# Performance work log

Hardware: AMD Instinct MI355X
Metric: run time of the kernel (lower is better)

## Reference

```python
import jax, jax.numpy as jnp
import numpy as np

N = 100000   # nodes
E = 1600000  # edges
D = 128      # emb_dim == in_dim
L = 5        # num_layer
G = 128      # graphs in batch
T = 10       # num_tasks
NB = 4       # edge (bond) types
BN_EPS = 1e-5


def setup_inputs() -> dict:
    key = jax.random.key(0)
    ks = jax.random.split(key, 10)
    x = jax.random.normal(ks[0], (N, D), jnp.float32)
    edge_index = jax.random.randint(ks[1], (2, E), 0, N, dtype=jnp.int32)
    edge_attr = jax.random.randint(ks[2], (E,), 0, NB, dtype=jnp.int32)
    batch = jnp.sort(jax.random.randint(ks[3], (N,), 0, G, dtype=jnp.int32))
    # stacked per-layer params (layer 0 has in_dim == emb_dim == D)
    W = jax.random.normal(ks[4], (L, D, D), jnp.float32) * 0.05
    b = jnp.zeros((L, D), jnp.float32)
    root = jax.random.normal(ks[5], (L, D), jnp.float32) * 0.05   # root_emb.weight per layer
    bond = jax.random.normal(ks[6], (L, NB, D), jnp.float32) * 0.05  # bond encoder tables
    gamma = jnp.ones((L, D), jnp.float32)
    beta = jnp.zeros((L, D), jnp.float32)
    W_out = jax.random.normal(ks[7], (D, T), jnp.float32) * 0.05
    b_out = jnp.zeros((T,), jnp.float32)
    return {"x": x, "edge_index": edge_index, "edge_attr": edge_attr, "batch": batch,
            "W": W, "b": b, "root": root, "bond": bond, "gamma": gamma, "beta": beta,
            "W_out": W_out, "b_out": b_out}


def reference(x, edge_index, edge_attr, batch, W, b, root, bond, gamma, beta, W_out, b_out):
    row, col = edge_index[0], edge_index[1]
    # degree of source nodes (+1 self), symmetric-ish norm as in GCNConv.forward
    deg = jax.ops.segment_sum(jnp.ones((E,), x.dtype), row, num_segments=N) + 1.0  # [N]
    dinv = deg ** -0.5  # never inf since deg >= 1
    norm = dinv[row] * dinv[col]  # [E]
    h = x
    for l in range(L):
        hx = h @ W[l] + b[l]                                   # [N, D] linear
        ee = bond[l][edge_attr]                                # [E, D] edge embedding gather
        msg = norm[:, None] * jax.nn.relu(hx[row] + ee)        # [E, D] message
        agg = jax.ops.segment_sum(msg, col, num_segments=N)    # [N, D] scatter-add to targets
        h2 = agg + jax.nn.relu(hx + root[l]) / deg[:, None]    # self/root term
        # BatchNorm1d (training-mode batch stats, biased variance)
        mu = h2.mean(axis=0)
        var = h2.var(axis=0)
        h2 = (h2 - mu) * jax.lax.rsqrt(var + BN_EPS) * gamma[l] + beta[l]
        h = jax.nn.relu(h2)
    # global mean pool over graphs
    cnt = jnp.maximum(jax.ops.segment_sum(jnp.ones((N,), h.dtype), batch, num_segments=G), 1.0)
    hg = jax.ops.segment_sum(h, batch, num_segments=G) / cnt[:, None]  # [G, D]
    return hg @ W_out + b_out  # [G, T]
```

## Files before the change

### kernel.cpp

```cpp
#include <hip/hip_runtime.h>
#include <hip/hip_fp16.h>
#include <math.h>

#define N_NODES 100000
#define N_EDGES 1600000
#define DIM     128
#define NLAYER  5
#define NGRAPH  128
#define NTASK   10
#define NBOND   4
#define BN_EPS  1e-5f

__global__ __launch_bounds__(256) void hist_kernel(
    const int* __restrict__ row, const int* __restrict__ col,
    int* __restrict__ cnt_row, int* __restrict__ cnt_col) {
  int i = blockIdx.x * blockDim.x + threadIdx.x;
  int stride = gridDim.x * blockDim.x;
  for (; i < N_EDGES; i += stride) {
    atomicAdd(&cnt_row[row[i]], 1);
    atomicAdd(&cnt_col[col[i]], 1);
  }
}

__global__ __launch_bounds__(256) void deg_kernel(
    const int* __restrict__ cnt_row, float* __restrict__ deg, float* __restrict__ dinv) {
  int i = blockIdx.x * blockDim.x + threadIdx.x;
  if (i < N_NODES) {
    float d = (float)cnt_row[i] + 1.0f;
    deg[i] = d;
    dinv[i] = rsqrtf(d);
  }
}

__global__ __launch_bounds__(256) void scan1_kernel(
    const int* __restrict__ cnt, int* __restrict__ excl, int* __restrict__ bsum) {
  __shared__ int s[256];
  int t = threadIdx.x;
  int i = blockIdx.x * 256 + t;
  int v = (i < N_NODES) ? cnt[i] : 0;
  s[t] = v;
  __syncthreads();
  for (int off = 1; off < 256; off <<= 1) {
    int add = (t >= off) ? s[t - off] : 0;
    __syncthreads();
    s[t] += add;
    __syncthreads();
  }
  if (i < N_NODES) excl[i] = s[t] - v;
  if (t == 255) bsum[blockIdx.x] = s[255];
}

__global__ __launch_bounds__(512) void scan2_kernel(
    const int* __restrict__ bsum, int* __restrict__ bexcl, int nb) {
  __shared__ int s[512];
  int t = threadIdx.x;
  int v = (t < nb) ? bsum[t] : 0;
  s[t] = v;
  __syncthreads();
  for (int off = 1; off < 512; off <<= 1) {
    int add = (t >= off) ? s[t - off] : 0;
    __syncthreads();
    s[t] += add;
    __syncthreads();
  }
  if (t < nb) bexcl[t] = s[t] - v;
}

__global__ __launch_bounds__(256) void scan3_kernel(
    int* __restrict__ excl, const int* __restrict__ bexcl) {
  int i = blockIdx.x * 256 + threadIdx.x;
  if (i < N_NODES) excl[i] += bexcl[blockIdx.x];
  if (i == 0) excl[N_NODES] = N_EDGES;
}

__global__ __launch_bounds__(256) void scatter_kernel(
    const int* __restrict__ row, const int* __restrict__ col,
    const int* __restrict__ attr, const int* __restrict__ csr_off,
    int* __restrict__ pos, const float* __restrict__ dinv,
    int* __restrict__ src_pack, float* __restrict__ enorm) {
  int e = blockIdx.x * blockDim.x + threadIdx.x;
  int stride = gridDim.x * blockDim.x;
  for (; e < N_EDGES; e += stride) {
    int d = col[e];
    int s = row[e];
    int p = csr_off[d] + atomicAdd(&pos[d], 1);
    src_pack[p] = s | (attr[e] << 20);
    enorm[p] = dinv[s] * dinv[d];
  }
}

__device__ __forceinline__ void bn_coeff(float s, float q, float g, float b,
                                         float& sc, float& sh) {
  const float invN = 1.0f / (float)N_NODES;
  float mu = s * invN;
  float ex2 = q * invN;
  float var = ex2 - mu * mu;
  float inv = rsqrtf(var + BN_EPS);
  sc = g * inv;
  sh = fmaf(-mu, sc, b);
}

__device__ __forceinline__ void bn_coeff4(float4 s, float4 q, float4 g, float4 b,
                                          float4& sc, float4& sh) {
  bn_coeff(s.x, q.x, g.x, b.x, sc.x, sh.x);
  bn_coeff(s.y, q.y, g.y, b.y, sc.y, sh.y);
  bn_coeff(s.z, q.z, g.z, b.z, sc.z, sh.z);
  bn_coeff(s.w, q.w, g.w, b.w, sc.w, sh.w);
}

#define GBM 128
__global__ __launch_bounds__(512, 4) void gemm_kernel(
    const float* __restrict__ hin, const float* __restrict__ W,
    const float* __restrict__ bias, const float* __restrict__ bnprev,
    const float* __restrict__ gammaL, const float* __restrict__ betaL,
    int useact, uint2* __restrict__ hxh, float* __restrict__ bnzero) {
  __shared__ float4 hs[128 * 8];
  __shared__ float4 Ws[32 * 32];
  int t = threadIdx.x;
  if (blockIdx.x == 0 && t < 256) bnzero[t] = 0.0f;
  int cg = t & 15;
  int rg = t >> 4;
  int cr = rg & 3;
  int slot = t & 7;
  int srow = t >> 3;
  int sswz = slot ^ (srow & 3);
  int r0 = blockIdx.x * GBM;
  if (r0 > N_NODES - GBM) r0 = N_NODES - GBM;

  const float4* hg = (const float4*)hin;
  const float4* wg = (const float4*)W;
  const float4* bs4 = (const float4*)bnprev;
  const float4* g4 = (const float4*)gammaL;
  const float4* b4 = (const float4*)betaL;

  float acc0[4][4], acc1[4][4];
  {
    float b0[4], b1[4];
#pragma unroll
    for (int j = 0; j < 4; j++) {
      b0[j] = bias[4 * cg + j];
      b1[j] = bias[64 + 4 * cg + j];
    }
#pragma unroll
    for (int i = 0; i < 4; i++)
#pragma unroll
      for (int j = 0; j < 4; j++) { acc0[i][j] = b0[j]; acc1[i][j] = b1[j]; }
  }

  float4 psc, psh;
  if (useact) {
    float4 s4 = bs4[slot], q4 = bs4[32 + slot];
    bn_coeff4(s4, q4, g4[slot], b4[slot], psc, psh);
  }
  float4 ph0 = hg[(size_t)(r0 + srow) * 32 + slot];
  float4 ph1 = hg[(size_t)(r0 + srow + 64) * 32 + slot];
  float4 pw0 = wg[t];
  float4 pw1 = wg[512 + t];

#pragma unroll 1
  for (int p = 0; p < 4; ++p) {
    float4 v0 = ph0, v1 = ph1;
    if (useact) {
      v0.x = fmaxf(fmaf(v0.x, psc.x, psh.x), 0.f);
      v0.y = fmaxf(fmaf(v0.y, psc.y, psh.y), 0.f);
      v0.z = fmaxf(fmaf(v0.z, psc.z, psh.z), 0.f);
      v0.w = fmaxf(fmaf(v0.w, psc.w, psh.w), 0.f);
      v1.x = fmaxf(fmaf(v1.x, psc.x, psh.x), 0.f);
      v1.y = fmaxf(fmaf(v1.y, psc.y, psh.y), 0.f);
      v1.z = fmaxf(fmaf(v1.z, psc.z, psh.z), 0.f);
      v1.w = fmaxf(fmaf(v1.w, psc.w, psh.w), 0.f);
    }
    hs[srow * 8 + sswz] = v0;
    hs[(srow + 64) * 8 + sswz] = v1;
    Ws[t] = pw0;
    Ws[512 + t] = pw1;
    __syncthreads();
    if (p < 3) {
      if (useact) {
        float4 s4 = bs4[(p + 1) * 8 + slot], q4 = bs4[32 + (p + 1) * 8 + slot];
        bn_coeff4(s4, q4, g4[(p + 1) * 8 + slot], b4[(p + 1) * 8 + slot], psc, psh);
      }
      ph0 = hg[(size_t)(r0 + srow) * 32 + (p + 1) * 8 + slot];
      ph1 = hg[(size_t)(r0 + srow + 64) * 32 + (p + 1) * 8 + slot];
      pw0 = wg[(p + 1) * 1024 + t];
      pw1 = wg[(p + 1) * 1024 + 512 + t];
    }
#pragma unroll 1
    for (int k4 = 0; k4 < 8; k4++) {
      float4 w0[4], w1[4];
#pragma unroll
      for (int kk = 0; kk < 4; kk++) {
        w0[kk] = Ws[(k4 * 4 + kk) * 32 + cg];
        w1[kk] = Ws[(k4 * 4 + kk) * 32 + 16 + cg];
      }
      int soff = k4 ^ cr;
#pragma unroll
      for (int i = 0; i < 4; i++) {
        float4 hf = hs[(rg + 32 * i) * 8 + soff];
#pragma unroll
        for (int kk = 0; kk < 4; kk++) {
          float hv = ((const float*)&hf)[kk];
          acc0[i][0] = fmaf(hv, w0[kk].x, acc0[i][0]);
          acc0[i][1] = fmaf(hv, w0[kk].y, acc0[i][1]);
          acc0[i][2] = fmaf(hv, w0[kk].z, acc0[i][2]);
          acc0[i][3] = fmaf(hv, w0[kk].w, acc0[i][3]);
          acc1[i][0] = fmaf(hv, w1[kk].x, acc1[i][0]);
          acc1[i][1] = fmaf(hv, w1[kk].y, acc1[i][1]);
          acc1[i][2] = fmaf(hv, w1[kk].z, acc1[i][2]);
          acc1[i][3] = fmaf(hv, w1[kk].w, acc1[i][3]);
        }
      }
    }
    __syncthreads();
  }
#pragma unroll
  for (int i = 0; i < 4; i++) {
    int grow = r0 + rg + 32 * i;
    __half2 a01 = __floats2half2_rn(acc0[i][0], acc0[i][1]);
    __half2 a23 = __floats2half2_rn(acc0[i][2], acc0[i][3]);
    __half2 c01 = __floats2half2_rn(acc1[i][0], acc1[i][1]);
    __half2 c23 = __floats2half2_rn(acc1[i][2], acc1[i][3]);
    uint2 u0, u1;
    u0.x = __builtin_bit_cast(unsigned int, a01);
    u0.y = __builtin_bit_cast(unsigned int, a23);
    u1.x = __builtin_bit_cast(unsigned int, c01);
    u1.y = __builtin_bit_cast(unsigned int, c23);
    hxh[(size_t)grow * 32 + cg] = u0;
    hxh[(size_t)grow * 32 + 16 + cg] = u1;
  }
}

__global__ __launch_bounds__(256) void agg_kernel(
    const uint2* __restrict__ hxh, const int* __restrict__ csr_off,
    const int* __restrict__ src_pack, const float* __restrict__ enorm,
    const float* __restrict__ bond, const float* __restrict__ root,
    const float* __restrict__ deg, float* __restrict__ h2,
    float* __restrict__ bnbuf) {
  __shared__ float4 bondS[NBOND * 32];
  __shared__ float4 rootS[32];
  __shared__ float sbn[256];
  int t = threadIdx.x;
  if (t < NBOND * 32) bondS[t] = ((const float4*)bond)[t];
  if (t < 32) rootS[t] = ((const float4*)root)[t];
  sbn[t] = 0.0f;
  __syncthreads();

  int lane = t & 63;
  int laneq = lane & 31;
  int half = lane >> 5;
  int wid = t >> 6;
  int gw = blockIdx.x * 4 + wid;
  int nw = gridDim.x * 4;
  float4* h24 = (float4*)h2;

  float s0 = 0.f, s1 = 0.f, s2 = 0.f, s3 = 0.f;
  float q0 = 0.f, q1 = 0.f, q2 = 0.f, q3 = 0.f;
  for (int n = gw; n < N_NODES; n += nw) {
    int e0 = csr_off[n], e1 = csr_off[n + 1];
    float a0 = 0.f, a1 = 0.f, a2 = 0.f, a3 = 0.f;
    int e = e0 + half;
    for (; e + 6 < e1; e += 8) {
      int sp0 = src_pack[e];
      int sp1 = src_pack[e + 2];
      int sp2 = src_pack[e + 4];
      int sp3 = src_pack[e + 6];
      float nr0 = enorm[e];
      float nr1 = enorm[e + 2];
      float nr2 = enorm[e + 4];
      float nr3 = enorm[e + 6];
      uint2 u0 = hxh[(size_t)(sp0 & 0xFFFFF) * 32 + laneq];
      uint2 u1 = hxh[(size_t)(sp1 & 0xFFFFF) * 32 + laneq];
      uint2 u2 = hxh[(size_t)(sp2 & 0xFFFFF) * 32 + laneq];
      uint2 u3 = hxh[(size_t)(sp3 & 0xFFFFF) * 32 + laneq];
      float4 b0 = bondS[(sp0 >> 20) * 32 + laneq];
      float4 b1 = bondS[(sp1 >> 20) * 32 + laneq];
      float4 b2 = bondS[(sp2 >> 20) * 32 + laneq];
      float4 b3 = bondS[(sp3 >> 20) * 32 + laneq];
      float2 v0a = __half22float2(__builtin_bit_cast(__half2, u0.x));
      float2 v0b = __half22float2(__builtin_bit_cast(__half2, u0.y));
      float2 v1a = __half22float2(__builtin_bit_cast(__half2, u1.x));
      float2 v1b = __half22float2(__builtin_bit_cast(__half2, u1.y));
      float2 v2a = __half22float2(__builtin_bit_cast(__half2, u2.x));
      float2 v2b = __half22float2(__builtin_bit_cast(__half2, u2.y));
      float2 v3a = __half22float2(__builtin_bit_cast(__half2, u3.x));
      float2 v3b = __half22float2(__builtin_bit_cast(__half2, u3.y));
      a0 = fmaf(nr0, fmaxf(v0a.x + b0.x, 0.f), a0);
      a1 = fmaf(nr0, fmaxf(v0a.y + b0.y, 0.f), a1);
      a2 = fmaf(nr0, fmaxf(v0b.x + b0.z, 0.f), a2);
      a3 = fmaf(nr0, fmaxf(v0b.y + b0.w, 0.f), a3);
      a0 = fmaf(nr1, fmaxf(v1a.x + b1.x, 0.f), a0);
      a1 = fmaf(nr1, fmaxf(v1a.y + b1.y, 0.f), a1);
      a2 = fmaf(nr1, fmaxf(v1b.x + b1.z, 0.f), a2);
      a3 = fmaf(nr1, fmaxf(v1b.y + b1.w, 0.f), a3);
      a0 = fmaf(nr2, fmaxf(v2a.x + b2.x, 0.f), a0);
      a1 = fmaf(nr2, fmaxf(v2a.y + b2.y, 0.f), a1);
      a2 = fmaf(nr2, fmaxf(v2b.x + b2.z, 0.f), a2);
      a3 = fmaf(nr2, fmaxf(v2b.y + b2.w, 0.f), a3);
      a0 = fmaf(nr3, fmaxf(v3a.x + b3.x, 0.f), a0);
      a1 = fmaf(nr3, fmaxf(v3a.y + b3.y, 0.f), a1);
      a2 = fmaf(nr3, fmaxf(v3b.x + b3.z, 0.f), a2);
      a3 = fmaf(nr3, fmaxf(v3b.y + b3.w, 0.f), a3);
    }
    for (; e < e1; e += 2) {
      int sp = src_pack[e];
      float nrm = enorm[e];
      uint2 u = hxh[(size_t)(sp & 0xFFFFF) * 32 + laneq];
      float4 eb = bondS[(sp >> 20) * 32 + laneq];
      float2 va = __half22float2(__builtin_bit_cast(__half2, u.x));
      float2 vb = __half22float2(__builtin_bit_cast(__half2, u.y));
      a0 = fmaf(nrm, fmaxf(va.x + eb.x, 0.f), a0);
      a1 = fmaf(nrm, fmaxf(va.y + eb.y, 0.f), a1);
      a2 = fmaf(nrm, fmaxf(vb.x + eb.z, 0.f), a2);
      a3 = fmaf(nrm, fmaxf(vb.y + eb.w, 0.f), a3);
    }
    a0 += __shfl_xor(a0, 32, 64);
    a1 += __shfl_xor(a1, 32, 64);
    a2 += __shfl_xor(a2, 32, 64);
    a3 += __shfl_xor(a3, 32, 64);
    if (half == 0) {
      float inv = 1.0f / deg[n];
      uint2 u = hxh[(size_t)n * 32 + laneq];
      float2 va = __half22float2(__builtin_bit_cast(__half2, u.x));
      float2 vb = __half22float2(__builtin_bit_cast(__half2, u.y));
      float4 r = rootS[laneq];
      a0 += fmaxf(va.x + r.x, 0.f) * inv;
      a1 += fmaxf(va.y + r.y, 0.f) * inv;
      a2 += fmaxf(vb.x + r.z, 0.f) * inv;
      a3 += fmaxf(vb.y + r.w, 0.f) * inv;
      float4 o;
      o.x = a0; o.y = a1; o.z = a2; o.w = a3;
      h24[(size_t)n * 32 + laneq] = o;
      s0 += a0; s1 += a1; s2 += a2; s3 += a3;
      q0 += a0 * a0; q1 += a1 * a1; q2 += a2 * a2; q3 += a3 * a3;
    }
  }
  if (half == 0) {
    int f = 4 * laneq;
    atomicAdd(&sbn[f + 0], s0);
    atomicAdd(&sbn[f + 1], s1);
    atomicAdd(&sbn[f + 2], s2);
    atomicAdd(&sbn[f + 3], s3);
    atomicAdd(&sbn[128 + f + 0], q0);
    atomicAdd(&sbn[128 + f + 1], q1);
    atomicAdd(&sbn[128 + f + 2], q2);
    atomicAdd(&sbn[128 + f + 3], q3);
  }
  __syncthreads();
  atomicAdd(&bnbuf[t], sbn[t]);
}

__global__ __launch_bounds__(256) void pool_kernel(
    const float* __restrict__ h2, const int* __restrict__ batch,
    const float* __restrict__ bnlast, const float* __restrict__ gammaL,
    const float* __restrict__ betaL,
    float* __restrict__ pool, float* __restrict__ pcnt) {
  int t = threadIdx.x;
  int lane = t & 63;
  int wid = t >> 6;
  int gw = blockIdx.x * 4 + wid;
  int nw = gridDim.x * 4;
  int chunk = (N_NODES + nw - 1) / nw;
  int n0 = gw * chunk;
  int n1 = min(n0 + chunk, N_NODES);
  if (n0 >= N_NODES) return;
  const float2* h22 = (const float2*)h2;
  int f0 = 2 * lane, f1 = f0 + 1;
  float sc0, sh0, sc1, sh1;
  bn_coeff(bnlast[f0], bnlast[128 + f0], gammaL[f0], betaL[f0], sc0, sh0);
  bn_coeff(bnlast[f1], bnlast[128 + f1], gammaL[f1], betaL[f1], sc1, sh1);
  int curg = batch[n0];
  float a0 = 0.f, a1 = 0.f, c = 0.f;
  for (int n = n0; n < n1; n++) {
    int g = batch[n];
    if (g != curg) {
      atomicAdd(&pool[curg * DIM + f0], a0);
      atomicAdd(&pool[curg * DIM + f1], a1);
      if (lane == 0) atomicAdd(&pcnt[curg], c);
      a0 = a1 = c = 0.f;
      curg = g;
    }
    float2 v = h22[(size_t)n * 64 + lane];
    a0 += fmaxf(fmaf(v.x, sc0, sh0), 0.f);
    a1 += fmaxf(fmaf(v.y, sc1, sh1), 0.f);
    c += 1.0f;
  }
  atomicAdd(&pool[curg * DIM + f0], a0);
  atomicAdd(&pool[curg * DIM + f1], a1);
  if (lane == 0) atomicAdd(&pcnt[curg], c);
}

__global__ __launch_bounds__(256) void out_kernel(
    const float* __restrict__ pool, const float* __restrict__ pcnt,
    const float* __restrict__ Wout, const float* __restrict__ bout,
    float* __restrict__ out) {
  int idx = blockIdx.x * blockDim.x + threadIdx.x;
  if (idx >= NGRAPH * NTASK) return;
  int g = idx / NTASK, tt = idx % NTASK;
  float inv = 1.0f / fmaxf(pcnt[g], 1.0f);
  float acc = bout[tt];
  for (int d = 0; d < DIM; d++)
    acc = fmaf(pool[g * DIM + d] * inv, Wout[d * NTASK + tt], acc);
  out[idx] = acc;
}

extern "C" void kernel_launch(void* const* d_in, const int* in_sizes, int n_in,
                              void* d_out, int out_size, void* d_ws, size_t ws_size,
                              hipStream_t stream) {
  const float* x     = (const float*)d_in[0];
  const int*   eidx  = (const int*)d_in[1];
  const int*   row   = eidx;
  const int*   col   = eidx + N_EDGES;
  const int*   eattr = (const int*)d_in[2];
  const int*   batch = (const int*)d_in[3];
  const float* W     = (const float*)d_in[4];
  const float* b     = (const float*)d_in[5];
  const float* root  = (const float*)d_in[6];
  const float* bond  = (const float*)d_in[7];
  const float* gamma = (const float*)d_in[8];
  const float* beta  = (const float*)d_in[9];
  const float* Wout  = (const float*)d_in[10];
  const float* bout  = (const float*)d_in[11];
  float* out = (float*)d_out;

  char* w = (char*)d_ws;
  size_t off = 0;
  auto alloc = [&](size_t bytes) -> void* {
    void* p = w + off;
    off = (off + bytes + 511) & ~(size_t)511;
    return p;
  };
  int*   cnt_row = (int*)alloc(N_NODES * 4);
  int*   cnt_col = (int*)alloc(N_NODES * 4);
  int*   pos     = (int*)alloc(N_NODES * 4);
  float* pool    = (float*)alloc(NGRAPH * DIM * 4);
  float* pcnt    = (float*)alloc(NGRAPH * 4);
  size_t zbytes  = off;
  int*   csr     = (int*)alloc((N_NODES + 1) * 4);
  int*   bsum    = (int*)alloc(512 * 4);
  int*   bexcl   = (int*)alloc(512 * 4);
  float* deg     = (float*)alloc(N_NODES * 4);
  float* dinv    = (float*)alloc(N_NODES * 4);
  int*   spck    = (int*)alloc((size_t)N_EDGES * 4);
  float* enorm   = (float*)alloc((size_t)N_EDGES * 4);
  uint2* hxh     = (uint2*)alloc((size_t)N_NODES * DIM * 2);
  float* hA      = (float*)alloc((size_t)N_NODES * DIM * 4);
  float* hB      = (float*)alloc((size_t)N_NODES * DIM * 4);
  float* bnbufA  = (float*)alloc(256 * 4);
  float* bnbufB  = (float*)alloc(256 * 4);

  hipMemsetAsync(d_ws, 0, zbytes, stream);

  hist_kernel<<<2048, 256, 0, stream>>>(row, col, cnt_row, cnt_col);
  deg_kernel<<<(N_NODES + 255) / 256, 256, 0, stream>>>(cnt_row, deg, dinv);
  const int nb = (N_NODES + 255) / 256;
  scan1_kernel<<<nb, 256, 0, stream>>>(cnt_col, csr, bsum);
  scan2_kernel<<<1, 512, 0, stream>>>(bsum, bexcl, nb);
  scan3_kernel<<<nb, 256, 0, stream>>>(csr, bexcl);
  scatter_kernel<<<2048, 256, 0, stream>>>(row, col, eattr, csr, pos, dinv, spck, enorm);

  const int gblocks = (N_NODES + GBM - 1) / GBM;
  const float* hin = x;
  for (int l = 0; l < NLAYER; l++) {
    float* h2      = (l % 2 == 0) ? hA : hB;
    float* bufcur  = (l % 2 == 0) ? bnbufA : bnbufB;
    float* bufprev = (l % 2 == 0) ? bnbufB : bnbufA;
    gemm_kernel<<<gblocks, 512, 0, stream>>>(
        hin, W + (size_t)l * DIM * DIM, b + l * DIM,
        bufprev, gamma + (size_t)(l > 0 ? l - 1 : 0) * DIM,
        beta + (size_t)(l > 0 ? l - 1 : 0) * DIM,
        (l > 0) ? 1 : 0, hxh, bufcur);
    agg_kernel<<<2048, 256, 0, stream>>>(
        hxh, csr, spck, enorm, bond + (size_t)l * NBOND * DIM, root + l * DIM,
        deg, h2, bufcur);
    hin = h2;
  }
  pool_kernel<<<256, 256, 0, stream>>>(hin, batch, bnbufA,
                                       gamma + 4 * DIM, beta + 4 * DIM, pool, pcnt);
  out_kernel<<<5, 256, 0, stream>>>(pool, pcnt, Wout, bout, out);
}
```

Measured before the change: 1.224 ms.

## Fuse layer-0 GEMM with edge histogram, merge deg into scan, pack edge metadata

```diff
diff --git a/kernel.cpp b/kernel.cpp
--- a/kernel.cpp
+++ b/kernel.cpp
@@ -11,32 +11,17 @@
 #define NBOND   4
 #define BN_EPS  1e-5f
 
-__global__ __launch_bounds__(256) void hist_kernel(
-    const int* __restrict__ row, const int* __restrict__ col,
-    int* __restrict__ cnt_row, int* __restrict__ cnt_col) {
-  int i = blockIdx.x * blockDim.x + threadIdx.x;
-  int stride = gridDim.x * blockDim.x;
-  for (; i < N_EDGES; i += stride) {
-    atomicAdd(&cnt_row[row[i]], 1);
-    atomicAdd(&cnt_col[col[i]], 1);
-  }
-}
-
-__global__ __launch_bounds__(256) void deg_kernel(
+__global__ __launch_bounds__(256) void scan1_kernel(
+    const int* __restrict__ cnt, int* __restrict__ excl, int* __restrict__ bsum,
     const int* __restrict__ cnt_row, float* __restrict__ deg, float* __restrict__ dinv) {
-  int i = blockIdx.x * blockDim.x + threadIdx.x;
+  __shared__ int s[256];
+  int t = threadIdx.x;
+  int i = blockIdx.x * 256 + t;
   if (i < N_NODES) {
     float d = (float)cnt_row[i] + 1.0f;
     deg[i] = d;
     dinv[i] = rsqrtf(d);
   }
-}
-
-__global__ __launch_bounds__(256) void scan1_kernel(
-    const int* __restrict__ cnt, int* __restrict__ excl, int* __restrict__ bsum) {
-  __shared__ int s[256];
-  int t = threadIdx.x;
-  int i = blockIdx.x * 256 + t;
   int v = (i < N_NODES) ? cnt[i] : 0;
   s[t] = v;
   __syncthreads();
@@ -77,15 +62,17 @@
     const int* __restrict__ row, const int* __restrict__ col,
     const int* __restrict__ attr, const int* __restrict__ csr_off,
     int* __restrict__ pos, const float* __restrict__ dinv,
-    int* __restrict__ src_pack, float* __restrict__ enorm) {
+    int2* __restrict__ emeta) {
   int e = blockIdx.x * blockDim.x + threadIdx.x;
   int stride = gridDim.x * blockDim.x;
   for (; e < N_EDGES; e += stride) {
     int d = col[e];
     int s = row[e];
     int p = csr_off[d] + atomicAdd(&pos[d], 1);
-    src_pack[p] = s | (attr[e] << 20);
-    enorm[p] = dinv[s] * dinv[d];
+    int2 m;
+    m.x = s | (attr[e] << 20);
+    m.y = __float_as_int(dinv[s] * dinv[d]);
+    emeta[p] = m;
   }
 }
 
@@ -109,22 +96,20 @@
 }
 
 #define GBM 128
-__global__ __launch_bounds__(512, 4) void gemm_kernel(
+template<int USEACT>
+__device__ __forceinline__ void gemm_body(
     const float* __restrict__ hin, const float* __restrict__ W,
     const float* __restrict__ bias, const float* __restrict__ bnprev,
     const float* __restrict__ gammaL, const float* __restrict__ betaL,
-    int useact, uint2* __restrict__ hxh, float* __restrict__ bnzero) {
-  __shared__ float4 hs[128 * 8];
-  __shared__ float4 Ws[32 * 32];
-  int t = threadIdx.x;
-  if (blockIdx.x == 0 && t < 256) bnzero[t] = 0.0f;
+    uint2* __restrict__ hxh, float4* hs, float4* Ws, int bid) {
+  int t = threadIdx.x;
   int cg = t & 15;
   int rg = t >> 4;
   int cr = rg & 3;
   int slot = t & 7;
   int srow = t >> 3;
   int sswz = slot ^ (srow & 3);
-  int r0 = blockIdx.x * GBM;
+  int r0 = bid * GBM;
   if (r0 > N_NODES - GBM) r0 = N_NODES - GBM;
 
   const float4* hg = (const float4*)hin;
@@ -148,9 +133,8 @@
   }
 
   float4 psc, psh;
-  if (useact) {
-    float4 s4 = bs4[slot], q4 = bs4[32 + slot];
-    bn_coeff4(s4, q4, g4[slot], b4[slot], psc, psh);
+  if (USEACT) {
+    bn_coeff4(bs4[slot], bs4[32 + slot], g4[slot], b4[slot], psc, psh);
   }
   float4 ph0 = hg[(size_t)(r0 + srow) * 32 + slot];
   float4 ph1 = hg[(size_t)(r0 + srow + 64) * 32 + slot];
@@ -160,7 +144,7 @@
 #pragma unroll 1
   for (int p = 0; p < 4; ++p) {
     float4 v0 = ph0, v1 = ph1;
-    if (useact) {
+    if (USEACT) {
       v0.x = fmaxf(fmaf(v0.x, psc.x, psh.x), 0.f);
       v0.y = fmaxf(fmaf(v0.y, psc.y, psh.y), 0.f);
       v0.z = fmaxf(fmaf(v0.z, psc.z, psh.z), 0.f);
@@ -176,9 +160,9 @@
     Ws[512 + t] = pw1;
     __syncthreads();
     if (p < 3) {
-      if (useact) {
-        float4 s4 = bs4[(p + 1) * 8 + slot], q4 = bs4[32 + (p + 1) * 8 + slot];
-        bn_coeff4(s4, q4, g4[(p + 1) * 8 + slot], b4[(p + 1) * 8 + slot], psc, psh);
+      if (USEACT) {
+        bn_coeff4(bs4[(p + 1) * 8 + slot], bs4[32 + (p + 1) * 8 + slot],
+                  g4[(p + 1) * 8 + slot], b4[(p + 1) * 8 + slot], psc, psh);
       }
       ph0 = hg[(size_t)(r0 + srow) * 32 + (p + 1) * 8 + slot];
       ph1 = hg[(size_t)(r0 + srow + 64) * 32 + (p + 1) * 8 + slot];
@@ -230,9 +214,42 @@
   }
 }
 
+__global__ __launch_bounds__(512, 4) void gemm_kernel(
+    const float* __restrict__ hin, const float* __restrict__ W,
+    const float* __restrict__ bias, const float* __restrict__ bnprev,
+    const float* __restrict__ gammaL, const float* __restrict__ betaL,
+    uint2* __restrict__ hxh, float* __restrict__ bnzero) {
+  __shared__ float4 hs[128 * 8];
+  __shared__ float4 Ws[32 * 32];
+  if (blockIdx.x == 0 && threadIdx.x < 256) bnzero[threadIdx.x] = 0.0f;
+  gemm_body<1>(hin, W, bias, bnprev, gammaL, betaL, hxh, hs, Ws, blockIdx.x);
+}
+
+__global__ __launch_bounds__(512, 4) void gemm0_hist_kernel(
+    const float* __restrict__ x, const float* __restrict__ W,
+    const float* __restrict__ bias, uint2* __restrict__ hxh,
+    float* __restrict__ bnzero,
+    const int* __restrict__ row, const int* __restrict__ col,
+    int* __restrict__ cnt_row, int* __restrict__ cnt_col, int gblocks) {
+  __shared__ float4 hs[128 * 8];
+  __shared__ float4 Ws[32 * 32];
+  int t = threadIdx.x;
+  if ((int)blockIdx.x >= gblocks) {
+    int i = ((int)blockIdx.x - gblocks) * 512 + t;
+    int stride = ((int)gridDim.x - gblocks) * 512;
+    for (; i < N_EDGES; i += stride) {
+      atomicAdd(&cnt_row[row[i]], 1);
+      atomicAdd(&cnt_col[col[i]], 1);
+    }
+    return;
+  }
+  if (blockIdx.x == 0 && t < 256) bnzero[t] = 0.0f;
+  gemm_body<0>(x, W, bias, nullptr, nullptr, nullptr, hxh, hs, Ws, blockIdx.x);
+}
+
 __global__ __launch_bounds__(256) void agg_kernel(
     const uint2* __restrict__ hxh, const int* __restrict__ csr_off,
-    const int* __restrict__ src_pack, const float* __restrict__ enorm,
+    const int2* __restrict__ emeta,
     const float* __restrict__ bond, const float* __restrict__ root,
     const float* __restrict__ deg, float* __restrict__ h2,
     float* __restrict__ bnbuf) {
@@ -260,22 +277,22 @@
     float a0 = 0.f, a1 = 0.f, a2 = 0.f, a3 = 0.f;
     int e = e0 + half;
     for (; e + 6 < e1; e += 8) {
-      int sp0 = src_pack[e];
-      int sp1 = src_pack[e + 2];
-      int sp2 = src_pack[e + 4];
-      int sp3 = src_pack[e + 6];
-      float nr0 = enorm[e];
-      float nr1 = enorm[e + 2];
-      float nr2 = enorm[e + 4];
-      float nr3 = enorm[e + 6];
-      uint2 u0 = hxh[(size_t)(sp0 & 0xFFFFF) * 32 + laneq];
-      uint2 u1 = hxh[(size_t)(sp1 & 0xFFFFF) * 32 + laneq];
-      uint2 u2 = hxh[(size_t)(sp2 & 0xFFFFF) * 32 + laneq];
-      uint2 u3 = hxh[(size_t)(sp3 & 0xFFFFF) * 32 + laneq];
-      float4 b0 = bondS[(sp0 >> 20) * 32 + laneq];
-      float4 b1 = bondS[(sp1 >> 20) * 32 + laneq];
-      float4 b2 = bondS[(sp2 >> 20) * 32 + laneq];
-      float4 b3 = bondS[(sp3 >> 20) * 32 + laneq];
+      int2 m0 = emeta[e];
+      int2 m1 = emeta[e + 2];
+      int2 m2 = emeta[e + 4];
+      int2 m3 = emeta[e + 6];
+      float nr0 = __int_as_float(m0.y);
+      float nr1 = __int_as_float(m1.y);
+      float nr2 = __int_as_float(m2.y);
+      float nr3 = __int_as_float(m3.y);
+      uint2 u0 = hxh[(size_t)(m0.x & 0xFFFFF) * 32 + laneq];
+      uint2 u1 = hxh[(size_t)(m1.x & 0xFFFFF) * 32 + laneq];
+      uint2 u2 = hxh[(size_t)(m2.x & 0xFFFFF) * 32 + laneq];
+      uint2 u3 = hxh[(size_t)(m3.x & 0xFFFFF) * 32 + laneq];
+      float4 b0 = bondS[(m0.x >> 20) * 32 + laneq];
+      float4 b1 = bondS[(m1.x >> 20) * 32 + laneq];
+      float4 b2 = bondS[(m2.x >> 20) * 32 + laneq];
+      float4 b3 = bondS[(m3.x >> 20) * 32 + laneq];
       float2 v0a = __half22float2(__builtin_bit_cast(__half2, u0.x));
       float2 v0b = __half22float2(__builtin_bit_cast(__half2, u0.y));
       float2 v1a = __half22float2(__builtin_bit_cast(__half2, u1.x));
@@ -302,10 +319,10 @@
       a3 = fmaf(nr3, fmaxf(v3b.y + b3.w, 0.f), a3);
     }
     for (; e < e1; e += 2) {
-      int sp = src_pack[e];
-      float nrm = enorm[e];
-      uint2 u = hxh[(size_t)(sp & 0xFFFFF) * 32 + laneq];
-      float4 eb = bondS[(sp >> 20) * 32 + laneq];
+      int2 m = emeta[e];
+      float nrm = __int_as_float(m.y);
+      uint2 u = hxh[(size_t)(m.x & 0xFFFFF) * 32 + laneq];
+      float4 eb = bondS[(m.x >> 20) * 32 + laneq];
       float2 va = __half22float2(__builtin_bit_cast(__half2, u.x));
       float2 vb = __half22float2(__builtin_bit_cast(__half2, u.y));
       a0 = fmaf(nrm, fmaxf(va.x + eb.x, 0.f), a0);
@@ -440,8 +457,7 @@
   int*   bexcl   = (int*)alloc(512 * 4);
   float* deg     = (float*)alloc(N_NODES * 4);
   float* dinv    = (float*)alloc(N_NODES * 4);
-  int*   spck    = (int*)alloc((size_t)N_EDGES * 4);
-  float* enorm   = (float*)alloc((size_t)N_EDGES * 4);
+  int2*  emeta   = (int2*)alloc((size_t)N_EDGES * 8);
   uint2* hxh     = (uint2*)alloc((size_t)N_NODES * DIM * 2);
   float* hA      = (float*)alloc((size_t)N_NODES * DIM * 4);
   float* hB      = (float*)alloc((size_t)N_NODES * DIM * 4);
@@ -450,27 +466,30 @@
 
   hipMemsetAsync(d_ws, 0, zbytes, stream);
 
-  hist_kernel<<<2048, 256, 0, stream>>>(row, col, cnt_row, cnt_col);
-  deg_kernel<<<(N_NODES + 255) / 256, 256, 0, stream>>>(cnt_row, deg, dinv);
+  const int gblocks = (N_NODES + GBM - 1) / GBM;
+  gemm0_hist_kernel<<<gblocks + 512, 512, 0, stream>>>(
+      x, W, b, hxh, bnbufA, row, col, cnt_row, cnt_col, gblocks);
+
   const int nb = (N_NODES + 255) / 256;
-  scan1_kernel<<<nb, 256, 0, stream>>>(cnt_col, csr, bsum);
+  scan1_kernel<<<nb, 256, 0, stream>>>(cnt_col, csr, bsum, cnt_row, deg, dinv);
   scan2_kernel<<<1, 512, 0, stream>>>(bsum, bexcl, nb);
   scan3_kernel<<<nb, 256, 0, stream>>>(csr, bexcl);
-  scatter_kernel<<<2048, 256, 0, stream>>>(row, col, eattr, csr, pos, dinv, spck, enorm);
-
-  const int gblocks = (N_NODES + GBM - 1) / GBM;
-  const float* hin = x;
-  for (int l = 0; l < NLAYER; l++) {
+  scatter_kernel<<<2048, 256, 0, stream>>>(row, col, eattr, csr, pos, dinv, emeta);
+
+  agg_kernel<<<2048, 256, 0, stream>>>(
+      hxh, csr, emeta, bond, root, deg, hA, bnbufA);
+
+  const float* hin = hA;
+  for (int l = 1; l < NLAYER; l++) {
     float* h2      = (l % 2 == 0) ? hA : hB;
     float* bufcur  = (l % 2 == 0) ? bnbufA : bnbufB;
     float* bufprev = (l % 2 == 0) ? bnbufB : bnbufA;
     gemm_kernel<<<gblocks, 512, 0, stream>>>(
         hin, W + (size_t)l * DIM * DIM, b + l * DIM,
-        bufprev, gamma + (size_t)(l > 0 ? l - 1 : 0) * DIM,
-        beta + (size_t)(l > 0 ? l - 1 : 0) * DIM,
-        (l > 0) ? 1 : 0, hxh, bufcur);
+        bufprev, gamma + (size_t)(l - 1) * DIM, beta + (size_t)(l - 1) * DIM,
+        hxh, bufcur);
     agg_kernel<<<2048, 256, 0, stream>>>(
-        hxh, csr, spck, enorm, bond + (size_t)l * NBOND * DIM, root + l * DIM,
+        hxh, csr, emeta, bond + (size_t)l * NBOND * DIM, root + l * DIM,
         deg, h2, bufcur);
     hin = h2;
   }
```

Result: slower. 1.298 ms (+6.0%).
